# Performance work log

Measured on AMD Instinct MI355X. Metric: run time of the kernel, lower is better.

## Reference

```python
import jax, jax.numpy as jnp
import numpy as np

B, S, H = 8, 2048, 768      # batch, seq_len, hidden_size
N = 512                     # spans per example
MAXW = 30                   # max span width (length in [0, MAXW-1] -> width <= MAXW)


def setup_inputs() -> dict:
    key = jax.random.key(0)
    k1, k2, k3, k4 = jax.random.split(key, 4)
    embeddings = jax.random.normal(k1, (B, S, H), dtype=jnp.float32)
    starts = jax.random.randint(k2, (B, N), 0, S - MAXW)          # span starts
    lengths = jax.random.randint(k3, (B, N), 0, MAXW)             # end = start + length
    w = jax.random.normal(k4, (H, 1), dtype=jnp.float32) * 0.02   # nn.Linear(hidden, 1) weight (transposed)
    b = jnp.zeros((1,), dtype=jnp.float32)                        # linear bias
    return {"embeddings": embeddings, "w": w, "b": b, "starts": starts, "lengths": lengths}


def reference(embeddings, w, b, starts, lengths):
    # Vectorized ragged span pooling: gather up to MAXW tokens per span,
    # masked softmax over attention scores, then concat [start, end, attn].
    ends = starts + lengths                                  # inclusive end index
    offs = jnp.arange(MAXW)                                  # (W,)
    positions = starts[..., None] + offs                     # (B, N, W)
    mask = offs[None, None, :] <= lengths[..., None]         # (B, N, W) valid-token mask

    gather = jax.vmap(lambda e, p: e[p])                     # per-example gather
    span_emb = gather(embeddings, positions)                 # (B, N, W, H)

    scores = span_emb @ w + b                                # (B, N, W, 1)
    scores = jnp.where(mask[..., None], scores, -jnp.inf)
    attn_w = jax.nn.softmax(scores, axis=2)                  # masked softmax over span width
    attn_out = jnp.sum(attn_w * span_emb, axis=2)            # (B, N, H)

    start_emb = gather(embeddings, starts)                   # (B, N, H)
    end_emb = gather(embeddings, ends)                       # (B, N, H)
    return jnp.concatenate([start_emb, end_emb, attn_out], axis=-1)  # (B, N, 3H)
```

## Files before the change

### kernel.cpp

```cpp
#include <hip/hip_runtime.h>
#include <hip/hip_bf16.h>
#include <math.h>

#define BB 8
#define SS 2048
#define HH 768
#define NN 512
#define MAXW 30

static __device__ __forceinline__ unsigned short f2bf(float f) {
    union { float f; unsigned int u; } v; v.f = f;
    unsigned int r = (v.u + 0x7FFFu + ((v.u >> 16) & 1u)) >> 16;
    return (unsigned short)r;
}
static __device__ __forceinline__ float bflo(unsigned int u) {
    union { unsigned int u; float f; } v; v.u = u << 16; return v.f;
}
static __device__ __forceinline__ float bfhi(unsigned int u) {
    union { unsigned int u; float f; } v; v.u = u & 0xFFFF0000u; return v.f;
}

__global__ __launch_bounds__(256) void conv_kernel(
    const float* __restrict__ emb,
    const float* __restrict__ w,
    const float* __restrict__ bias,
    unsigned short* __restrict__ ebf,
    float*       __restrict__ scores)
{
    const int tid  = threadIdx.x;
    const int wv   = tid >> 6;
    const int lane = tid & 63;
    const int bi   = blockIdx.x & 7;
    const int g    = (int)blockIdx.x >> 3;
    const int t0   = g * 16 + wv * 4;

    const float* eb = emb + (size_t)bi * SS * HH;
    unsigned short* ob = ebf + (size_t)bi * SS * HH;

    const int h0 = lane * 4;
    const float4 w0 = *reinterpret_cast<const float4*>(w + h0);
    const float4 w1 = *reinterpret_cast<const float4*>(w + h0 + 256);
    const float4 w2 = *reinterpret_cast<const float4*>(w + h0 + 512);
    const float bb = bias[0];

    #pragma unroll
    for (int k = 0; k < 4; ++k) {
        const int t = t0 + k;
        const float* rp = eb + (size_t)t * HH;
        float4 v0 = *reinterpret_cast<const float4*>(rp + h0);
        float4 v1 = *reinterpret_cast<const float4*>(rp + h0 + 256);
        float4 v2 = *reinterpret_cast<const float4*>(rp + h0 + 512);

        float d = v0.x * w0.x + v0.y * w0.y + v0.z * w0.z + v0.w * w0.w
                + v1.x * w1.x + v1.y * w1.y + v1.z * w1.z + v1.w * w1.w
                + v2.x * w2.x + v2.y * w2.y + v2.z * w2.z + v2.w * w2.w;
        #pragma unroll
        for (int off = 32; off; off >>= 1) d += __shfl_xor(d, off);

        uint2 pa, pb, pc;
        pa.x = (unsigned)f2bf(v0.x) | ((unsigned)f2bf(v0.y) << 16);
        pa.y = (unsigned)f2bf(v0.z) | ((unsigned)f2bf(v0.w) << 16);
        pb.x = (unsigned)f2bf(v1.x) | ((unsigned)f2bf(v1.y) << 16);
        pb.y = (unsigned)f2bf(v1.z) | ((unsigned)f2bf(v1.w) << 16);
        pc.x = (unsigned)f2bf(v2.x) | ((unsigned)f2bf(v2.y) << 16);
        pc.y = (unsigned)f2bf(v2.z) | ((unsigned)f2bf(v2.w) << 16);

        unsigned short* op = ob + (size_t)t * HH;
        *reinterpret_cast<uint2*>(op + h0)       = pa;
        *reinterpret_cast<uint2*>(op + h0 + 256) = pb;
        *reinterpret_cast<uint2*>(op + h0 + 512) = pc;

        if (lane == 0) scores[bi * SS + t] = d + bb;
    }
}

__global__ __launch_bounds__(256) void span_bf16_kernel(
    const unsigned short* __restrict__ ebf,
    const float* __restrict__ scores,
    const int*   __restrict__ starts,
    const int*   __restrict__ lengths,
    float*       __restrict__ out)
{
    const int tid  = threadIdx.x;
    const int wv   = tid >> 6;
    const int lane = tid & 63;
    const int bi   = blockIdx.x & 7;
    const int rank = ((int)blockIdx.x >> 3) * 4 + wv;
    const int span = bi * NN + rank;

    const int start = starts[span];
    const int len   = lengths[span];

    float sc = (lane <= len) ? scores[bi * SS + start + lane] : -INFINITY;
    float m = sc;
    #pragma unroll
    for (int off = 32; off; off >>= 1) m = fmaxf(m, __shfl_xor(m, off));
    float e = (lane <= len) ? __expf(sc - m) : 0.f;
    float sum = e;
    #pragma unroll
    for (int off = 32; off; off >>= 1) sum += __shfl_xor(sum, off);
    const float p = e / sum;

    const unsigned short* rb = ebf + (size_t)bi * SS * HH + (size_t)start * HH;
    const int h0 = lane * 4;
    float* orow = out + (size_t)span * (3 * HH);

    float4 a0 = make_float4(0.f, 0.f, 0.f, 0.f), a1 = a0, a2 = a0;

    const unsigned short* rp0 = rb;
    uint2 cA = *reinterpret_cast<const uint2*>(rp0 + h0);
    uint2 cB = *reinterpret_cast<const uint2*>(rp0 + h0 + 256);
    uint2 cC = *reinterpret_cast<const uint2*>(rp0 + h0 + 512);
    const unsigned short* rp1 = rb + (size_t)min(1, len) * HH;
    uint2 xA = *reinterpret_cast<const uint2*>(rp1 + h0);
    uint2 xB = *reinterpret_cast<const uint2*>(rp1 + h0 + 256);
    uint2 xC = *reinterpret_cast<const uint2*>(rp1 + h0 + 512);

    for (int t = 0; t <= len; ++t) {
        const unsigned short* rp2 = rb + (size_t)min(t + 2, len) * HH;
        uint2 yA = *reinterpret_cast<const uint2*>(rp2 + h0);
        uint2 yB = *reinterpret_cast<const uint2*>(rp2 + h0 + 256);
        uint2 yC = *reinterpret_cast<const uint2*>(rp2 + h0 + 512);

        const float pt = __shfl(p, t);

        float4 f0, f1, f2;
        f0.x = bflo(cA.x); f0.y = bfhi(cA.x); f0.z = bflo(cA.y); f0.w = bfhi(cA.y);
        f1.x = bflo(cB.x); f1.y = bfhi(cB.x); f1.z = bflo(cB.y); f1.w = bfhi(cB.y);
        f2.x = bflo(cC.x); f2.y = bfhi(cC.x); f2.z = bflo(cC.y); f2.w = bfhi(cC.y);

        a0.x += pt * f0.x; a0.y += pt * f0.y; a0.z += pt * f0.z; a0.w += pt * f0.w;
        a1.x += pt * f1.x; a1.y += pt * f1.y; a1.z += pt * f1.z; a1.w += pt * f1.w;
        a2.x += pt * f2.x; a2.y += pt * f2.y; a2.z += pt * f2.z; a2.w += pt * f2.w;

        if (t == 0) {
            *reinterpret_cast<float4*>(orow + h0)       = f0;
            *reinterpret_cast<float4*>(orow + h0 + 256) = f1;
            *reinterpret_cast<float4*>(orow + h0 + 512) = f2;
        }
        if (t == len) {
            *reinterpret_cast<float4*>(orow + HH + h0)       = f0;
            *reinterpret_cast<float4*>(orow + HH + h0 + 256) = f1;
            *reinterpret_cast<float4*>(orow + HH + h0 + 512) = f2;
        }

        cA = xA; cB = xB; cC = xC;
        xA = yA; xB = yB; xC = yC;
    }

    *reinterpret_cast<float4*>(orow + 2 * HH + h0)       = a0;
    *reinterpret_cast<float4*>(orow + 2 * HH + h0 + 256) = a1;
    *reinterpret_cast<float4*>(orow + 2 * HH + h0 + 512) = a2;
}

__global__ __launch_bounds__(256) void span_fused_fp32_kernel(
    const float* __restrict__ emb, const float* __restrict__ w,
    const float* __restrict__ bias, const int* __restrict__ starts,
    const int* __restrict__ lengths, float* __restrict__ out)
{
    const int tid  = threadIdx.x;
    const int wv   = tid >> 6;
    const int lane = tid & 63;
    const int bi   = blockIdx.x & 7;
    const int rank = ((int)blockIdx.x >> 3) * 4 + wv;
    const int span = bi * NN + rank;
    const int start = starts[span];
    const int len   = lengths[span];

    const float* ebase = emb + (size_t)bi * SS * HH + (size_t)start * HH;
    const int h0 = lane * 4;
    float* orow = out + (size_t)span * (3 * HH);

    const float4 w0 = *reinterpret_cast<const float4*>(w + h0);
    const float4 w1 = *reinterpret_cast<const float4*>(w + h0 + 256);
    const float4 w2 = *reinterpret_cast<const float4*>(w + h0 + 512);
    const float bb = bias[0];

    float m = -INFINITY, ssum = 0.f;
    float4 a0 = make_float4(0.f, 0.f, 0.f, 0.f), a1 = a0, a2 = a0;

    const float* row = ebase;
    float4 v0 = *reinterpret_cast<const float4*>(row + h0);
    float4 v1 = *reinterpret_cast<const float4*>(row + h0 + 256);
    float4 v2 = *reinterpret_cast<const float4*>(row + h0 + 512);

    for (int t = 0; t <= len; ++t) {
        float4 n0, n1, n2;
        if (t < len) {
            const float* nr = row + HH;
            n0 = *reinterpret_cast<const float4*>(nr + h0);
            n1 = *reinterpret_cast<const float4*>(nr + h0 + 256);
            n2 = *reinterpret_cast<const float4*>(nr + h0 + 512);
        }
        float d = v0.x * w0.x + v0.y * w0.y + v0.z * w0.z + v0.w * w0.w
                + v1.x * w1.x + v1.y * w1.y + v1.z * w1.z + v1.w * w1.w
                + v2.x * w2.x + v2.y * w2.y + v2.z * w2.z + v2.w * w2.w;
        #pragma unroll
        for (int off = 32; off; off >>= 1) d += __shfl_xor(d, off);
        d += bb;
        if (d > m) {
            const float c = __expf(m - d);
            ssum *= c;
            a0.x *= c; a0.y *= c; a0.z *= c; a0.w *= c;
            a1.x *= c; a1.y *= c; a1.z *= c; a1.w *= c;
            a2.x *= c; a2.y *= c; a2.z *= c; a2.w *= c;
            m = d;
        }
        const float pt = __expf(d - m);
        ssum += pt;
        a0.x += pt * v0.x; a0.y += pt * v0.y; a0.z += pt * v0.z; a0.w += pt * v0.w;
        a1.x += pt * v1.x; a1.y += pt * v1.y; a1.z += pt * v1.z; a1.w += pt * v1.w;
        a2.x += pt * v2.x; a2.y += pt * v2.y; a2.z += pt * v2.z; a2.w += pt * v2.w;
        if (t == 0) {
            *reinterpret_cast<float4*>(orow + h0)       = v0;
            *reinterpret_cast<float4*>(orow + h0 + 256) = v1;
            *reinterpret_cast<float4*>(orow + h0 + 512) = v2;
        }
        if (t == len) {
            *reinterpret_cast<float4*>(orow + HH + h0)       = v0;
            *reinterpret_cast<float4*>(orow + HH + h0 + 256) = v1;
            *reinterpret_cast<float4*>(orow + HH + h0 + 512) = v2;
        }
        v0 = n0; v1 = n1; v2 = n2;
        row += HH;
    }
    const float inv = 1.f / ssum;
    a0.x *= inv; a0.y *= inv; a0.z *= inv; a0.w *= inv;
    a1.x *= inv; a1.y *= inv; a1.z *= inv; a1.w *= inv;
    a2.x *= inv; a2.y *= inv; a2.z *= inv; a2.w *= inv;
    *reinterpret_cast<float4*>(orow + 2 * HH + h0)       = a0;
    *reinterpret_cast<float4*>(orow + 2 * HH + h0 + 256) = a1;
    *reinterpret_cast<float4*>(orow + 2 * HH + h0 + 512) = a2;
}

extern "C" void kernel_launch(void* const* d_in, const int* in_sizes, int n_in,
                              void* d_out, int out_size, void* d_ws, size_t ws_size,
                              hipStream_t stream) {
    const float* emb     = (const float*)d_in[0];
    const float* w       = (const float*)d_in[1];
    const float* bias    = (const float*)d_in[2];
    const int*   starts  = (const int*)d_in[3];
    const int*   lengths = (const int*)d_in[4];
    float*       out     = (float*)d_out;

    const size_t ebf_bytes    = (size_t)BB * SS * HH * sizeof(unsigned short);
    const size_t scores_bytes = (size_t)BB * SS * sizeof(float);

    if (ws_size >= ebf_bytes + scores_bytes) {
        unsigned short* ebf = (unsigned short*)d_ws;
        float* scores = (float*)((char*)d_ws + ebf_bytes);

        conv_kernel<<<dim3(1024), dim3(256), 0, stream>>>(emb, w, bias, ebf, scores);
        span_bf16_kernel<<<dim3(BB * NN / 4), dim3(256), 0, stream>>>(
            ebf, scores, starts, lengths, out);
    } else {
        span_fused_fp32_kernel<<<dim3(BB * NN / 4), dim3(256), 0, stream>>>(
            emb, w, bias, starts, lengths, out);
    }
}
```

Before: 32.38 us.

## Sort spans by start position, add nontemporal loads/stores, skip redundant clamped loads

The prep kernel gets extra blocks that counting-sort each example's spans by start index into an order array. The span kernel then processes spans in that order, reversed, so that neighbouring waves gather overlapping token rows, which should improve L2 reuse. The conversion pass now uses nontemporal loads, the output writes use nontemporal stores, and the clamped prefetch loads beyond the span length are replaced by conditional loads. The costs are a small extra workspace buffer, LDS atomics in the sort blocks, and one more indirection per span.

```diff
diff --git a/kernel.cpp b/kernel.cpp
--- a/kernel.cpp
+++ b/kernel.cpp
@@ -8,6 +8,8 @@
 #define NN 512
 #define MAXW 30
 
+typedef float f32x4 __attribute__((ext_vector_type(4)));
+
 static __device__ __forceinline__ unsigned short f2bf(float f) {
     union { float f; unsigned int u; } v; v.f = f;
     unsigned int r = (v.u + 0x7FFFu + ((v.u >> 16) & 1u)) >> 16;
@@ -20,57 +22,101 @@
     union { unsigned int u; float f; } v; v.u = u & 0xFFFF0000u; return v.f;
 }
 
-__global__ __launch_bounds__(256) void conv_kernel(
+__global__ __launch_bounds__(256) void prep_kernel(
     const float* __restrict__ emb,
     const float* __restrict__ w,
     const float* __restrict__ bias,
+    const int*   __restrict__ starts,
     unsigned short* __restrict__ ebf,
-    float*       __restrict__ scores)
+    float*       __restrict__ scores,
+    int*         __restrict__ order)
 {
-    const int tid  = threadIdx.x;
-    const int wv   = tid >> 6;
-    const int lane = tid & 63;
-    const int bi   = blockIdx.x & 7;
-    const int g    = (int)blockIdx.x >> 3;
-    const int t0   = g * 16 + wv * 4;
-
-    const float* eb = emb + (size_t)bi * SS * HH;
-    unsigned short* ob = ebf + (size_t)bi * SS * HH;
-
-    const int h0 = lane * 4;
-    const float4 w0 = *reinterpret_cast<const float4*>(w + h0);
-    const float4 w1 = *reinterpret_cast<const float4*>(w + h0 + 256);
-    const float4 w2 = *reinterpret_cast<const float4*>(w + h0 + 512);
-    const float bb = bias[0];
-
-    #pragma unroll
-    for (int k = 0; k < 4; ++k) {
-        const int t = t0 + k;
-        const float* rp = eb + (size_t)t * HH;
-        float4 v0 = *reinterpret_cast<const float4*>(rp + h0);
-        float4 v1 = *reinterpret_cast<const float4*>(rp + h0 + 256);
-        float4 v2 = *reinterpret_cast<const float4*>(rp + h0 + 512);
-
-        float d = v0.x * w0.x + v0.y * w0.y + v0.z * w0.z + v0.w * w0.w
-                + v1.x * w1.x + v1.y * w1.y + v1.z * w1.z + v1.w * w1.w
-                + v2.x * w2.x + v2.y * w2.y + v2.z * w2.z + v2.w * w2.w;
-        #pragma unroll
-        for (int off = 32; off; off >>= 1) d += __shfl_xor(d, off);
-
-        uint2 pa, pb, pc;
-        pa.x = (unsigned)f2bf(v0.x) | ((unsigned)f2bf(v0.y) << 16);
-        pa.y = (unsigned)f2bf(v0.z) | ((unsigned)f2bf(v0.w) << 16);
-        pb.x = (unsigned)f2bf(v1.x) | ((unsigned)f2bf(v1.y) << 16);
-        pb.y = (unsigned)f2bf(v1.z) | ((unsigned)f2bf(v1.w) << 16);
-        pc.x = (unsigned)f2bf(v2.x) | ((unsigned)f2bf(v2.y) << 16);
-        pc.y = (unsigned)f2bf(v2.z) | ((unsigned)f2bf(v2.w) << 16);
-
-        unsigned short* op = ob + (size_t)t * HH;
-        *reinterpret_cast<uint2*>(op + h0)       = pa;
-        *reinterpret_cast<uint2*>(op + h0 + 256) = pb;
-        *reinterpret_cast<uint2*>(op + h0 + 512) = pc;
-
-        if (lane == 0) scores[bi * SS + t] = d + bb;
+    const int tid = threadIdx.x;
+
+    if ((int)blockIdx.x < 1024) {
+        const int wv   = tid >> 6;
+        const int lane = tid & 63;
+        const int bi   = blockIdx.x & 7;
+        const int g    = (int)blockIdx.x >> 3;
+        const int t0   = g * 16 + wv * 4;
+
+        const float* eb = emb + (size_t)bi * SS * HH;
+        unsigned short* ob = ebf + (size_t)bi * SS * HH;
+
+        const int h0 = lane * 4;
+        const f32x4 w0 = *reinterpret_cast<const f32x4*>(w + h0);
+        const f32x4 w1 = *reinterpret_cast<const f32x4*>(w + h0 + 256);
+        const f32x4 w2 = *reinterpret_cast<const f32x4*>(w + h0 + 512);
+        const float bb = bias[0];
+
+        #pragma unroll
+        for (int k = 0; k < 4; ++k) {
+            const int t = t0 + k;
+            const float* rp = eb + (size_t)t * HH;
+            f32x4 v0 = __builtin_nontemporal_load(reinterpret_cast<const f32x4*>(rp + h0));
+            f32x4 v1 = __builtin_nontemporal_load(reinterpret_cast<const f32x4*>(rp + h0 + 256));
+            f32x4 v2 = __builtin_nontemporal_load(reinterpret_cast<const f32x4*>(rp + h0 + 512));
+
+            float d = v0[0]*w0[0] + v0[1]*w0[1] + v0[2]*w0[2] + v0[3]*w0[3]
+                    + v1[0]*w1[0] + v1[1]*w1[1] + v1[2]*w1[2] + v1[3]*w1[3]
+                    + v2[0]*w2[0] + v2[1]*w2[1] + v2[2]*w2[2] + v2[3]*w2[3];
+            #pragma unroll
+            for (int off = 32; off; off >>= 1) d += __shfl_xor(d, off);
+
+            uint2 pa, pb, pc;
+            pa.x = (unsigned)f2bf(v0[0]) | ((unsigned)f2bf(v0[1]) << 16);
+            pa.y = (unsigned)f2bf(v0[2]) | ((unsigned)f2bf(v0[3]) << 16);
+            pb.x = (unsigned)f2bf(v1[0]) | ((unsigned)f2bf(v1[1]) << 16);
+            pb.y = (unsigned)f2bf(v1[2]) | ((unsigned)f2bf(v1[3]) << 16);
+            pc.x = (unsigned)f2bf(v2[0]) | ((unsigned)f2bf(v2[1]) << 16);
+            pc.y = (unsigned)f2bf(v2[2]) | ((unsigned)f2bf(v2[3]) << 16);
+
+            unsigned short* op = ob + (size_t)t * HH;
+            *reinterpret_cast<uint2*>(op + h0)       = pa;
+            *reinterpret_cast<uint2*>(op + h0 + 256) = pb;
+            *reinterpret_cast<uint2*>(op + h0 + 512) = pc;
+
+            if (lane == 0) scores[bi * SS + t] = d + bb;
+        }
+    } else {
+        const int b = blockIdx.x - 1024;
+        __shared__ int hist[SS];
+        __shared__ int wsum[4];
+
+        for (int i = tid; i < SS; i += 256) hist[i] = 0;
+        __syncthreads();
+
+        const int* st = starts + b * NN;
+        for (int n = tid; n < NN; n += 256) atomicAdd(&hist[st[n]], 1);
+        __syncthreads();
+
+        const int base = tid * 8;
+        int cnt[8]; int s = 0;
+        #pragma unroll
+        for (int k = 0; k < 8; ++k) { cnt[k] = hist[base + k]; s += cnt[k]; }
+
+        const int lane = tid & 63, wv = tid >> 6;
+        int v = s;
+        #pragma unroll
+        for (int off = 1; off < 64; off <<= 1) {
+            int u = __shfl_up(v, off);
+            if (lane >= off) v += u;
+        }
+        if (lane == 63) wsum[wv] = v;
+        __syncthreads();
+        int wbase = 0;
+        #pragma unroll
+        for (int k = 0; k < 4; ++k) wbase += (k < wv) ? wsum[k] : 0;
+
+        int excl = wbase + v - s;
+        #pragma unroll
+        for (int k = 0; k < 8; ++k) { int c = cnt[k]; hist[base + k] = excl; excl += c; }
+        __syncthreads();
+
+        for (int n = tid; n < NN; n += 256) {
+            int pos = atomicAdd(&hist[st[n]], 1);
+            order[b * NN + pos] = n;
+        }
     }
 }
 
@@ -79,14 +125,17 @@
     const float* __restrict__ scores,
     const int*   __restrict__ starts,
     const int*   __restrict__ lengths,
+    const int*   __restrict__ order,
     float*       __restrict__ out)
 {
     const int tid  = threadIdx.x;
     const int wv   = tid >> 6;
     const int lane = tid & 63;
     const int bi   = blockIdx.x & 7;
-    const int rank = ((int)blockIdx.x >> 3) * 4 + wv;
-    const int span = bi * NN + rank;
+    const int r    = ((int)blockIdx.x >> 3) * 4 + wv;
+    const int rank = NN - 1 - r;
+    const int n    = order ? order[bi * NN + rank] : r;
+    const int span = bi * NN + n;
 
     const int start = starts[span];
     const int len   = lengths[span];
@@ -107,20 +156,25 @@
 
     float4 a0 = make_float4(0.f, 0.f, 0.f, 0.f), a1 = a0, a2 = a0;
 
-    const unsigned short* rp0 = rb;
-    uint2 cA = *reinterpret_cast<const uint2*>(rp0 + h0);
-    uint2 cB = *reinterpret_cast<const uint2*>(rp0 + h0 + 256);
-    uint2 cC = *reinterpret_cast<const uint2*>(rp0 + h0 + 512);
-    const unsigned short* rp1 = rb + (size_t)min(1, len) * HH;
-    uint2 xA = *reinterpret_cast<const uint2*>(rp1 + h0);
-    uint2 xB = *reinterpret_cast<const uint2*>(rp1 + h0 + 256);
-    uint2 xC = *reinterpret_cast<const uint2*>(rp1 + h0 + 512);
+    uint2 cA = *reinterpret_cast<const uint2*>(rb + h0);
+    uint2 cB = *reinterpret_cast<const uint2*>(rb + h0 + 256);
+    uint2 cC = *reinterpret_cast<const uint2*>(rb + h0 + 512);
+    uint2 xA, xB, xC;
+    if (len >= 1) {
+        const unsigned short* rp1 = rb + HH;
+        xA = *reinterpret_cast<const uint2*>(rp1 + h0);
+        xB = *reinterpret_cast<const uint2*>(rp1 + h0 + 256);
+        xC = *reinterpret_cast<const uint2*>(rp1 + h0 + 512);
+    } else { xA = cA; xB = cB; xC = cC; }
 
     for (int t = 0; t <= len; ++t) {
-        const unsigned short* rp2 = rb + (size_t)min(t + 2, len) * HH;
-        uint2 yA = *reinterpret_cast<const uint2*>(rp2 + h0);
-        uint2 yB = *reinterpret_cast<const uint2*>(rp2 + h0 + 256);
-        uint2 yC = *reinterpret_cast<const uint2*>(rp2 + h0 + 512);
+        uint2 yA, yB, yC;
+        if (t + 2 <= len) {
+            const unsigned short* rp2 = rb + (size_t)(t + 2) * HH;
+            yA = *reinterpret_cast<const uint2*>(rp2 + h0);
+            yB = *reinterpret_cast<const uint2*>(rp2 + h0 + 256);
+            yC = *reinterpret_cast<const uint2*>(rp2 + h0 + 512);
+        } else { yA = cA; yB = cB; yC = cC; }
 
         const float pt = __shfl(p, t);
 
@@ -134,23 +188,23 @@
         a2.x += pt * f2.x; a2.y += pt * f2.y; a2.z += pt * f2.z; a2.w += pt * f2.w;
 
         if (t == 0) {
-            *reinterpret_cast<float4*>(orow + h0)       = f0;
-            *reinterpret_cast<float4*>(orow + h0 + 256) = f1;
-            *reinterpret_cast<float4*>(orow + h0 + 512) = f2;
+            __builtin_nontemporal_store(*(const f32x4*)&f0, (f32x4*)(orow + h0));
+            __builtin_nontemporal_store(*(const f32x4*)&f1, (f32x4*)(orow + h0 + 256));
+            __builtin_nontemporal_store(*(const f32x4*)&f2, (f32x4*)(orow + h0 + 512));
         }
         if (t == len) {
-            *reinterpret_cast<float4*>(orow + HH + h0)       = f0;
-            *reinterpret_cast<float4*>(orow + HH + h0 + 256) = f1;
-            *reinterpret_cast<float4*>(orow + HH + h0 + 512) = f2;
+            __builtin_nontemporal_store(*(const f32x4*)&f0, (f32x4*)(orow + HH + h0));
+            __builtin_nontemporal_store(*(const f32x4*)&f1, (f32x4*)(orow + HH + h0 + 256));
+            __builtin_nontemporal_store(*(const f32x4*)&f2, (f32x4*)(orow + HH + h0 + 512));
         }
 
         cA = xA; cB = xB; cC = xC;
         xA = yA; xB = yB; xC = yC;
     }
 
-    *reinterpret_cast<float4*>(orow + 2 * HH + h0)       = a0;
-    *reinterpret_cast<float4*>(orow + 2 * HH + h0 + 256) = a1;
-    *reinterpret_cast<float4*>(orow + 2 * HH + h0 + 512) = a2;
+    __builtin_nontemporal_store(*(const f32x4*)&a0, (f32x4*)(orow + 2 * HH + h0));
+    __builtin_nontemporal_store(*(const f32x4*)&a1, (f32x4*)(orow + 2 * HH + h0 + 256));
+    __builtin_nontemporal_store(*(const f32x4*)&a2, (f32x4*)(orow + 2 * HH + h0 + 512));
 }
 
 __global__ __launch_bounds__(256) void span_fused_fp32_kernel(
@@ -245,14 +299,17 @@
 
     const size_t ebf_bytes    = (size_t)BB * SS * HH * sizeof(unsigned short);
     const size_t scores_bytes = (size_t)BB * SS * sizeof(float);
-
-    if (ws_size >= ebf_bytes + scores_bytes) {
+    const size_t order_bytes  = (size_t)BB * NN * sizeof(int);
+
+    if (ws_size >= ebf_bytes + scores_bytes + order_bytes) {
         unsigned short* ebf = (unsigned short*)d_ws;
         float* scores = (float*)((char*)d_ws + ebf_bytes);
-
-        conv_kernel<<<dim3(1024), dim3(256), 0, stream>>>(emb, w, bias, ebf, scores);
+        int*   order  = (int*)((char*)d_ws + ebf_bytes + scores_bytes);
+
+        prep_kernel<<<dim3(1024 + BB), dim3(256), 0, stream>>>(
+            emb, w, bias, starts, ebf, scores, order);
         span_bf16_kernel<<<dim3(BB * NN / 4), dim3(256), 0, stream>>>(
-            ebf, scores, starts, lengths, out);
+            ebf, scores, starts, lengths, order, out);
     } else {
         span_fused_fp32_kernel<<<dim3(BB * NN / 4), dim3(256), 0, stream>>>(
             emb, w, bias, starts, lengths, out);
```

After: 30.97 us (median of 2 runs). 4.3% less time.
